# Kernel optimization log

Hardware: AMD Instinct MI355X
Metric: run time of the kernel (lower is better)

Reference implementation:

```python
import jax, jax.numpy as jnp
import numpy as np

B, CIN, COUT, K, L = 16, 512, 512, 3, 8192
STRIDE, PAD, DIL = 1, 1, 1  # 'same' conv: Lout == L


def setup_inputs() -> dict:
    key = jax.random.key(0)
    k1, k2, k3 = jax.random.split(key, 3)
    x = jax.random.normal(k1, (B, CIN, L), dtype=jnp.float32)
    # int8 quantized weight stored as int32 for portability; values in [-128, 127]
    qweight = jax.random.randint(k2, (COUT, CIN, K), -128, 128, dtype=jnp.int32)
    scale = jnp.float32(0.01)  # per-tensor dequant scale (w_max / 127)
    bias = jax.random.normal(k3, (COUT,), dtype=jnp.float32)
    return {"x": x, "qweight": qweight, "scale": scale, "bias": bias}


def reference(x, qweight, scale, bias):
    # Dequantize: fp32 weight = int8 * scale (materialized every call, as in torch module)
    w = (qweight.astype(jnp.float32) * scale).astype(x.dtype)
    out = jax.lax.conv_general_dilated(
        x, w,
        window_strides=(STRIDE,),
        padding=[(PAD, PAD)],
        rhs_dilation=(DIL,),
        dimension_numbers=("NCH", "OIH", "NCH"),
        feature_group_count=1,
    )
    return out + bias.astype(x.dtype)[None, :, None]
```

## Files before the change

### kernel.cpp

```cpp
#include <hip/hip_runtime.h>
#include <hip/hip_bf16.h>

#define CIN   512
#define COUT  512
#define LEN   8192
#define NB    16
#define KW    3
#define PROWS 8200

#define WB_ELEMS (COUT * CIN * KW)
#define WB_BYTES ((size_t)WB_ELEMS * 2)
#define XS_BYTES ((size_t)NB * PROWS * CIN * 2)

#define BM2 256
#define BN2 256
#define BK3 64
#define NT  ((CIN / BK3) * KW)
#define TILE3 (BM2 * BK3 * 2)

typedef __attribute__((ext_vector_type(4))) float f32x4;
typedef __attribute__((ext_vector_type(8))) short bf16x8;

static __device__ __forceinline__ unsigned short f2bf(float f) {
    union { float f; unsigned u; } cv; cv.f = f;
    return (unsigned short)((cv.u + 0x7fffu + ((cv.u >> 16) & 1u)) >> 16);
}

__global__ __launch_bounds__(256) void wconv_kernel(const int* __restrict__ q,
                                                    unsigned short* __restrict__ wb) {
    int idx = blockIdx.x * 256 + threadIdx.x;
    if (idx >= WB_ELEMS) return;
    int co = idx / (KW * CIN);
    int r  = idx - co * (KW * CIN);
    int t  = r >> 9;
    int ci = r & 511;
    wb[idx] = f2bf((float)q[(co * CIN + ci) * KW + t]);
}

__global__ __launch_bounds__(256) void zpad_kernel(unsigned short* __restrict__ xs) {
    int i = blockIdx.x * 256 + threadIdx.x;
    if (i >= NB * 2 * CIN) return;
    int b  = i >> 10;
    int r  = (i >> 9) & 1;
    int ci = i & 511;
    size_t p = (size_t)b * PROWS + (r ? 8193 : 0);
    xs[p * CIN + ci] = 0;
}

__global__ __launch_bounds__(256) void xprep_kernel(const float* __restrict__ x,
                                                    unsigned short* __restrict__ xs) {
    __shared__ char T[64 * 132];
    int blk = blockIdx.x;
    int b   = blk >> 10;
    int ci0 = ((blk >> 7) & 7) * 64;
    int l0  = (blk & 127) * 64;
    int tid = threadIdx.x;

    const float* src = x + ((size_t)b * CIN + ci0) * LEN + l0;
    for (int i = tid; i < 64 * 16; i += 256) {
        int r = i >> 4, c4 = i & 15;
        f32x4 v = *(const f32x4*)(src + (size_t)r * LEN + c4 * 4);
        unsigned lo = (unsigned)f2bf(v[0]) | ((unsigned)f2bf(v[1]) << 16);
        unsigned hi = (unsigned)f2bf(v[2]) | ((unsigned)f2bf(v[3]) << 16);
        char* p = T + r * 132 + c4 * 8;
        *(unsigned*)p       = lo;
        *(unsigned*)(p + 4) = hi;
    }
    __syncthreads();
    unsigned short* dst = xs + ((size_t)b * PROWS + 1 + l0) * CIN + ci0;
    for (int i = tid; i < 64 * 8; i += 256) {
        int l = i >> 3, c8 = i & 7;
        union { bf16x8 v; unsigned short s[8]; } pk;
        #pragma unroll
        for (int j = 0; j < 8; ++j)
            pk.s[j] = *(const unsigned short*)(T + (c8 * 8 + j) * 132 + l * 2);
        *(bf16x8*)(dst + (size_t)l * CIN + c8 * 8) = pk.v;
    }
}

__global__ __launch_bounds__(512, 2) void conv_kernel(
    const unsigned short* __restrict__ xs,
    const unsigned short* __restrict__ wb,
    const float* __restrict__ scale_p,
    const float* __restrict__ bias,
    float* __restrict__ out)
{
    __shared__ char sA[2][TILE3];
    __shared__ char sB[2][TILE3];

    const int bid = blockIdx.x;
    const int logical = (bid & 7) * 128 + (bid >> 3);
    const int co_tile = logical & 1;
    const int l_tile  = logical >> 1;
    const int b   = l_tile >> 5;
    const int l0  = (l_tile & 31) * BN2;
    const int co0 = co_tile * BM2;

    const int tid  = threadIdx.x;
    const int lane = tid & 63;
    const int wid  = tid >> 6;
    const int wr   = wid >> 2;
    const int wc   = wid & 3;
    const int lhi  = lane >> 4;
    const int llo  = lane & 15;

    f32x4 acc[8][4] = {};

    const char* xsB = (const char*)(xs + ((size_t)b * PROWS + l0) * CIN);
    const char* wbB = (const char*)wb + (size_t)co0 * (KW * CIN * 2);

#define STAGEU(buf_, c_, u_) do {                                                            \
    int tap_ = (c_) % KW;  int ci0_ = ((c_) / KW) * BK3;                                     \
    int rowoff_ = ((u_) & 1) * 128;                                                          \
    const char* src0_; size_t rstride_; char* dst0_;                                         \
    if ((u_) < 2) { src0_ = xsB + ((size_t)(tap_ + rowoff_) * CIN + ci0_) * 2;               \
                    rstride_ = CIN * 2; dst0_ = &sB[buf_][rowoff_ * 128]; }                   \
    else          { src0_ = wbB + (size_t)rowoff_ * (KW * CIN * 2)                           \
                            + ((size_t)tap_ * CIN + ci0_) * 2;                               \
                    rstride_ = KW * CIN * 2; dst0_ = &sA[buf_][rowoff_ * 128]; }             \
    _Pragma("unroll")                                                                        \
    for (int kk_ = 0; kk_ < 2; ++kk_) {                                                      \
        int it_ = tid + kk_ * 512;                                                           \
        int r_ = it_ >> 3, q_ = it_ & 7;                                                     \
        __builtin_amdgcn_global_load_lds(                                                    \
            (const __attribute__((address_space(1))) unsigned int*)                          \
                (src0_ + (size_t)r_ * rstride_ + ((q_ * 16) ^ ((r_ & 7) << 4))),             \
            (__attribute__((address_space(3))) unsigned int*)(dst0_ + it_ * 16),             \
            16, 0, 0);                                                                       \
    } } while (0)

#define LDA(d_, buf_, mq_, k_) do { int row_ = (mq_) * 32 + wr * 16 + llo;                   \
    d_ = *(const bf16x8*)(&sA[buf_][0] + row_ * 128                                          \
                          + (((k_) * 64 + lhi * 16) ^ ((row_ & 7) << 4))); } while (0)
#define LDB(d_, buf_, n_, k_) do { int row_ = wc * 64 + (n_) * 16 + llo;                     \
    d_ = *(const bf16x8*)(&sB[buf_][0] + row_ * 128                                          \
                          + (((k_) * 64 + lhi * 16) ^ ((row_ & 7) << 4))); } while (0)

#define MFMA16(p_) do {                                                                      \
    __builtin_amdgcn_s_setprio(1);                                                           \
    acc[2*(p_)  ][0] = __builtin_amdgcn_mfma_f32_16x16x32_bf16(a0_, bB00, acc[2*(p_)  ][0],0,0,0); \
    acc[2*(p_)  ][1] = __builtin_amdgcn_mfma_f32_16x16x32_bf16(a0_, bB10, acc[2*(p_)  ][1],0,0,0); \
    acc[2*(p_)  ][2] = __builtin_amdgcn_mfma_f32_16x16x32_bf16(a0_, bB20, acc[2*(p_)  ][2],0,0,0); \
    acc[2*(p_)  ][3] = __builtin_amdgcn_mfma_f32_16x16x32_bf16(a0_, bB30, acc[2*(p_)  ][3],0,0,0); \
    acc[2*(p_)+1][0] = __builtin_amdgcn_mfma_f32_16x16x32_bf16(a2_, bB00, acc[2*(p_)+1][0],0,0,0); \
    acc[2*(p_)+1][1] = __builtin_amdgcn_mfma_f32_16x16x32_bf16(a2_, bB10, acc[2*(p_)+1][1],0,0,0); \
    acc[2*(p_)+1][2] = __builtin_amdgcn_mfma_f32_16x16x32_bf16(a2_, bB20, acc[2*(p_)+1][2],0,0,0); \
    acc[2*(p_)+1][3] = __builtin_amdgcn_mfma_f32_16x16x32_bf16(a2_, bB30, acc[2*(p_)+1][3],0,0,0); \
    acc[2*(p_)  ][0] = __builtin_amdgcn_mfma_f32_16x16x32_bf16(a1_, bB01, acc[2*(p_)  ][0],0,0,0); \
    acc[2*(p_)  ][1] = __builtin_amdgcn_mfma_f32_16x16x32_bf16(a1_, bB11, acc[2*(p_)  ][1],0,0,0); \
    acc[2*(p_)  ][2] = __builtin_amdgcn_mfma_f32_16x16x32_bf16(a1_, bB21, acc[2*(p_)  ][2],0,0,0); \
    acc[2*(p_)  ][3] = __builtin_amdgcn_mfma_f32_16x16x32_bf16(a1_, bB31, acc[2*(p_)  ][3],0,0,0); \
    acc[2*(p_)+1][0] = __builtin_amdgcn_mfma_f32_16x16x32_bf16(a3_, bB01, acc[2*(p_)+1][0],0,0,0); \
    acc[2*(p_)+1][1] = __builtin_amdgcn_mfma_f32_16x16x32_bf16(a3_, bB11, acc[2*(p_)+1][1],0,0,0); \
    acc[2*(p_)+1][2] = __builtin_amdgcn_mfma_f32_16x16x32_bf16(a3_, bB21, acc[2*(p_)+1][2],0,0,0); \
    acc[2*(p_)+1][3] = __builtin_amdgcn_mfma_f32_16x16x32_bf16(a3_, bB31, acc[2*(p_)+1][3],0,0,0); \
    __builtin_amdgcn_s_setprio(0);                                                           \
    } while (0)

#define BAR()    __builtin_amdgcn_s_barrier()
#define SCHED0() __builtin_amdgcn_sched_barrier(0)
#define LGKM0()  asm volatile("s_waitcnt lgkmcnt(0)" ::: "memory")

    STAGEU(0, 0, 0); STAGEU(0, 0, 1); STAGEU(0, 0, 2); STAGEU(0, 0, 3);
    asm volatile("s_waitcnt vmcnt(2)" ::: "memory");
    BAR();

    bf16x8 bB00, bB01, bB10, bB11, bB20, bB21, bB30, bB31;
    bf16x8 a0_, a1_, a2_, a3_;

    #pragma unroll 1
    for (int c = 0; c < NT - 1; ++c) {
        const int buf = c & 1, nb = buf ^ 1;
        SCHED0();
        LDB(bB00, buf, 0, 0); LDB(bB01, buf, 0, 1);
        LDB(bB10, buf, 1, 0); LDB(bB11, buf, 1, 1);
        LDB(bB20, buf, 2, 0); LDB(bB21, buf, 2, 1);
        LDB(bB30, buf, 3, 0); LDB(bB31, buf, 3, 1);
        LDA(a0_, buf, 0, 0); LDA(a1_, buf, 0, 1); LDA(a2_, buf, 1, 0); LDA(a3_, buf, 1, 1);
        STAGEU(nb, c + 1, 0);
        BAR(); LGKM0(); SCHED0();
        MFMA16(0);
        BAR();
        SCHED0();
        LDA(a0_, buf, 2, 0); LDA(a1_, buf, 2, 1); LDA(a2_, buf, 3, 0); LDA(a3_, buf, 3, 1);
        STAGEU(nb, c + 1, 1);
        asm volatile("s_waitcnt vmcnt(4)" ::: "memory");
        BAR(); LGKM0(); SCHED0();
        MFMA16(1);
        BAR();
        SCHED0();
        LDA(a0_, buf, 4, 0); LDA(a1_, buf, 4, 1); LDA(a2_, buf, 5, 0); LDA(a3_, buf, 5, 1);
        STAGEU(nb, c + 1, 2);
        BAR(); LGKM0(); SCHED0();
        MFMA16(2);
        BAR();
        SCHED0();
        LDA(a0_, buf, 6, 0); LDA(a1_, buf, 6, 1); LDA(a2_, buf, 7, 0); LDA(a3_, buf, 7, 1);
        STAGEU(nb, c + 1, 3);
        asm volatile("s_waitcnt vmcnt(2)" ::: "memory");
        BAR(); LGKM0(); SCHED0();
        MFMA16(3);
        BAR();
    }
    {
        const int buf = (NT - 1) & 1;
        SCHED0();
        LDB(bB00, buf, 0, 0); LDB(bB01, buf, 0, 1);
        LDB(bB10, buf, 1, 0); LDB(bB11, buf, 1, 1);
        LDB(bB20, buf, 2, 0); LDB(bB21, buf, 2, 1);
        LDB(bB30, buf, 3, 0); LDB(bB31, buf, 3, 1);
        LDA(a0_, buf, 0, 0); LDA(a1_, buf, 0, 1); LDA(a2_, buf, 1, 0); LDA(a3_, buf, 1, 1);
        BAR(); LGKM0(); SCHED0();
        MFMA16(0);
        BAR();
        SCHED0();
        LDA(a0_, buf, 2, 0); LDA(a1_, buf, 2, 1); LDA(a2_, buf, 3, 0); LDA(a3_, buf, 3, 1);
        asm volatile("s_waitcnt vmcnt(0)" ::: "memory");
        BAR(); LGKM0(); SCHED0();
        MFMA16(1);
        BAR();
        SCHED0();
        LDA(a0_, buf, 4, 0); LDA(a1_, buf, 4, 1); LDA(a2_, buf, 5, 0); LDA(a3_, buf, 5, 1);
        BAR(); LGKM0(); SCHED0();
        MFMA16(2);
        BAR();
        SCHED0();
        LDA(a0_, buf, 6, 0); LDA(a1_, buf, 6, 1); LDA(a2_, buf, 7, 0); LDA(a3_, buf, 7, 1);
        LGKM0(); SCHED0();
        MFMA16(3);
    }
#undef STAGEU
#undef LDA
#undef LDB
#undef MFMA16

    const float sc = scale_p[0];
    #pragma unroll
    for (int m = 0; m < 8; ++m) {
        #pragma unroll
        for (int j = 0; j < 4; ++j) {
            int co = co0 + m * 32 + wr * 16 + lhi * 4 + j;
            float bv = bias[co];
            size_t orow = ((size_t)b * COUT + co) * LEN + l0 + wc * 64;
            #pragma unroll
            for (int n = 0; n < 4; ++n)
                out[orow + n * 16 + llo] = sc * acc[m][n][j] + bv;
        }
    }
}

__global__ __launch_bounds__(256, 2) void conv_fb_kernel(
    const float* __restrict__ x,
    const unsigned short* __restrict__ wb,
    const float* __restrict__ scale_p,
    const float* __restrict__ bias,
    float* __restrict__ out)
{
    __shared__ char xT[132 * 128];
    const int bid = blockIdx.x;
    const int logical = (bid & 7) * 512 + (bid >> 3);
    const int co_tile = logical & 3;
    const int n_tile  = logical >> 2;
    const int b   = n_tile >> 6;
    const int l0  = (n_tile & 63) * 128;
    const int co0 = co_tile * 128;
    const int tid  = threadIdx.x;
    const int lane = tid & 63;
    const int wid  = tid >> 6;
    const int wr = wid >> 1, wc = wid & 1;
    const int lhi = lane >> 4;
    const int llo = lane & 15;
    f32x4 acc[4][4] = {};
    const float* xb = x + (size_t)b * CIN * LEN;

    for (int ci0 = 0; ci0 < CIN; ci0 += 64) {
        __syncthreads();
        for (int it = tid; it < 132 * 8; it += 256) {
            int c = it % 132;
            int o = it / 132;
            int l = l0 - 1 + c;
            float v[8];
            if (l >= 0 && l < LEN) {
                const float* src = xb + (size_t)(ci0 + o * 8) * LEN + l;
                #pragma unroll
                for (int j = 0; j < 8; ++j) v[j] = src[(size_t)j * LEN];
            } else {
                #pragma unroll
                for (int j = 0; j < 8; ++j) v[j] = 0.f;
            }
            union { bf16x8 v8; unsigned short s[8]; } pk;
            #pragma unroll
            for (int j = 0; j < 8; ++j) pk.s[j] = f2bf(v[j]);
            int byte = c * 128 + ((o * 16) ^ ((c & 7) << 4));
            *reinterpret_cast<bf16x8*>(xT + byte) = pk.v8;
        }
        __syncthreads();
        #pragma unroll
        for (int t = 0; t < KW; ++t) {
            #pragma unroll
            for (int s = 0; s < 2; ++s) {
                bf16x8 af[4];
                #pragma unroll
                for (int m = 0; m < 4; ++m)
                    af[m] = *reinterpret_cast<const bf16x8*>(
                        wb + (size_t)(co0 + wr * 64 + m * 16 + llo) * (KW * CIN)
                           + t * CIN + ci0 + s * 32 + 8 * lhi);
                bf16x8 bfr[4];
                #pragma unroll
                for (int n = 0; n < 4; ++n) {
                    int col = wc * 64 + n * 16 + llo + t;
                    int byte = col * 128 + (((s * 32 + 8 * lhi) * 2) ^ ((col & 7) << 4));
                    bfr[n] = *reinterpret_cast<const bf16x8*>(xT + byte);
                }
                #pragma unroll
                for (int m = 0; m < 4; ++m)
                    #pragma unroll
                    for (int n = 0; n < 4; ++n)
                        acc[m][n] = __builtin_amdgcn_mfma_f32_16x16x32_bf16(af[m], bfr[n], acc[m][n], 0, 0, 0);
            }
        }
    }
    const float sc = scale_p[0];
    #pragma unroll
    for (int m = 0; m < 4; ++m) {
        #pragma unroll
        for (int j = 0; j < 4; ++j) {
            int co = co0 + wr * 64 + m * 16 + lhi * 4 + j;
            float bv = bias[co];
            size_t orow = ((size_t)b * COUT + co) * LEN + l0 + wc * 64;
            #pragma unroll
            for (int n = 0; n < 4; ++n)
                out[orow + n * 16 + llo] = sc * acc[m][n][j] + bv;
        }
    }
}

extern "C" void kernel_launch(void* const* d_in, const int* in_sizes, int n_in,
                              void* d_out, int out_size, void* d_ws, size_t ws_size,
                              hipStream_t stream) {
    const float* x    = (const float*)d_in[0];
    const int*   qw   = (const int*)d_in[1];
    const float* sc   = (const float*)d_in[2];
    const float* bias = (const float*)d_in[3];
    float* out = (float*)d_out;
    unsigned short* wb = (unsigned short*)d_ws;

    wconv_kernel<<<(WB_ELEMS + 255) / 256, 256, 0, stream>>>(qw, wb);

    if (ws_size >= WB_BYTES + XS_BYTES) {
        unsigned short* xsw = (unsigned short*)((char*)d_ws + WB_BYTES);
        zpad_kernel<<<(NB * 2 * CIN + 255) / 256, 256, 0, stream>>>(xsw);
        xprep_kernel<<<NB * 8 * (LEN / 64), 256, 0, stream>>>(x, xsw);
        conv_kernel<<<(COUT / BM2) * (NB * LEN / BN2), 512, 0, stream>>>(xsw, wb, sc, bias, out);
    } else {
        conv_fb_kernel<<<4096, 256, 0, stream>>>(x, wb, sc, bias, out);
    }
}
```

Measured before the change: 297.4 us.

## Precompute swizzled LDS/global addresses, reorder MFMA K-halves, fold zero-pad into xprep

The conv main loop now precomputes per-thread global and LDS pointers with the XOR swizzle folded in once, and advances them by constant deltas per K-step instead of recomputing addresses in every stage. MFMA issue is reordered so each phase processes one K-half (32 elements) against four A fragments, which reduces live B registers from eight to a reusable set. The separate zero-padding kernel is removed and its writes are folded into xprep, saving one launch. The aim is lower VALU address overhead and register pressure in the hot loop, but the pointer-stepping arithmetic for tap wraparound must stay exactly correct.

```diff
diff --git a/kernel.cpp b/kernel.cpp
--- a/kernel.cpp
+++ b/kernel.cpp
@@ -37,16 +37,6 @@
     wb[idx] = f2bf((float)q[(co * CIN + ci) * KW + t]);
 }
 
-__global__ __launch_bounds__(256) void zpad_kernel(unsigned short* __restrict__ xs) {
-    int i = blockIdx.x * 256 + threadIdx.x;
-    if (i >= NB * 2 * CIN) return;
-    int b  = i >> 10;
-    int r  = (i >> 9) & 1;
-    int ci = i & 511;
-    size_t p = (size_t)b * PROWS + (r ? 8193 : 0);
-    xs[p * CIN + ci] = 0;
-}
-
 __global__ __launch_bounds__(256) void xprep_kernel(const float* __restrict__ x,
                                                     unsigned short* __restrict__ xs) {
     __shared__ char T[64 * 132];
@@ -55,6 +45,11 @@
     int ci0 = ((blk >> 7) & 7) * 64;
     int l0  = (blk & 127) * 64;
     int tid = threadIdx.x;
+
+    if (l0 == 0 && tid < 64)
+        xs[((size_t)b * PROWS + 0) * CIN + ci0 + tid] = 0;
+    if (l0 == (LEN - 64) && tid < 64)
+        xs[((size_t)b * PROWS + (LEN + 1)) * CIN + ci0 + tid] = 0;
 
     const float* src = x + ((size_t)b * CIN + ci0) * LEN + l0;
     for (int i = tid; i < 64 * 16; i += 256) {
@@ -109,51 +104,59 @@
     const char* xsB = (const char*)(xs + ((size_t)b * PROWS + l0) * CIN);
     const char* wbB = (const char*)wb + (size_t)co0 * (KW * CIN * 2);
 
-#define STAGEU(buf_, c_, u_) do {                                                            \
-    int tap_ = (c_) % KW;  int ci0_ = ((c_) / KW) * BK3;                                     \
-    int rowoff_ = ((u_) & 1) * 128;                                                          \
-    const char* src0_; size_t rstride_; char* dst0_;                                         \
-    if ((u_) < 2) { src0_ = xsB + ((size_t)(tap_ + rowoff_) * CIN + ci0_) * 2;               \
-                    rstride_ = CIN * 2; dst0_ = &sB[buf_][rowoff_ * 128]; }                   \
-    else          { src0_ = wbB + (size_t)rowoff_ * (KW * CIN * 2)                           \
-                            + ((size_t)tap_ * CIN + ci0_) * 2;                               \
-                    rstride_ = KW * CIN * 2; dst0_ = &sA[buf_][rowoff_ * 128]; }             \
-    _Pragma("unroll")                                                                        \
-    for (int kk_ = 0; kk_ < 2; ++kk_) {                                                      \
-        int it_ = tid + kk_ * 512;                                                           \
-        int r_ = it_ >> 3, q_ = it_ & 7;                                                     \
-        __builtin_amdgcn_global_load_lds(                                                    \
-            (const __attribute__((address_space(1))) unsigned int*)                          \
-                (src0_ + (size_t)r_ * rstride_ + ((q_ * 16) ^ ((r_ & 7) << 4))),             \
-            (__attribute__((address_space(3))) unsigned int*)(dst0_ + it_ * 16),             \
-            16, 0, 0);                                                                       \
-    } } while (0)
-
-#define LDA(d_, buf_, mq_, k_) do { int row_ = (mq_) * 32 + wr * 16 + llo;                   \
-    d_ = *(const bf16x8*)(&sA[buf_][0] + row_ * 128                                          \
-                          + (((k_) * 64 + lhi * 16) ^ ((row_ & 7) << 4))); } while (0)
-#define LDB(d_, buf_, n_, k_) do { int row_ = wc * 64 + (n_) * 16 + llo;                     \
-    d_ = *(const bf16x8*)(&sB[buf_][0] + row_ * 128                                          \
-                          + (((k_) * 64 + lhi * 16) ^ ((row_ & 7) << 4))); } while (0)
-
-#define MFMA16(p_) do {                                                                      \
+    const int it0 = tid, it1 = tid + 512;
+    const int r0 = it0 >> 3, r1 = it1 >> 3;
+    const int sw0 = ((it0 & 7) * 16) ^ ((r0 & 7) << 4);
+    const int sw1 = ((it1 & 7) * 16) ^ ((r1 & 7) << 4);
+    const char* pBs[4] = { xsB + r0 * 1024 + sw0,          xsB + r1 * 1024 + sw1,
+                           xsB + (128 + r0) * 1024 + sw0,  xsB + (128 + r1) * 1024 + sw1 };
+    const char* pAs[4] = { wbB + (size_t)r0 * 3072 + sw0,         wbB + (size_t)r1 * 3072 + sw1,
+                           wbB + (size_t)(128 + r0) * 3072 + sw0, wbB + (size_t)(128 + r1) * 3072 + sw1 };
+    const int d0 = tid * 16, d1 = d0 + 8192;
+
+    const int s10 = llo & 3, s2 = (llo >> 2) & 1;
+    const int constA = (wr * 16 + llo) * 128 + ((lhi ^ s10) << 4);
+    const int constB = (wc * 64 + llo) * 128 + ((lhi ^ s10) << 4);
+    const char* pA0b = &sA[0][0] + constA + (s2 ? 64 : 0);
+    const char* pA1b = &sA[0][0] + constA + (s2 ? 0 : 64);
+    const char* pB0b = &sB[0][0] + constB + (s2 ? 64 : 0);
+    const char* pB1b = &sB[0][0] + constB + (s2 ? 0 : 64);
+
+#define STAGEU(buf_, u_) do {                                                                \
+    const char* s0_; const char* s1_; char* dd_;                                             \
+    if ((u_) == 0)      { s0_ = pBs[0]; s1_ = pBs[1]; dd_ = &sB[buf_][0];     }              \
+    else if ((u_) == 1) { s0_ = pBs[2]; s1_ = pBs[3]; dd_ = &sB[buf_][16384]; }              \
+    else if ((u_) == 2) { s0_ = pAs[0]; s1_ = pAs[1]; dd_ = &sA[buf_][0];     }              \
+    else                { s0_ = pAs[2]; s1_ = pAs[3]; dd_ = &sA[buf_][16384]; }              \
+    __builtin_amdgcn_global_load_lds(                                                        \
+        (const __attribute__((address_space(1))) unsigned int*)s0_,                          \
+        (__attribute__((address_space(3))) unsigned int*)(dd_ + d0), 16, 0, 0);              \
+    __builtin_amdgcn_global_load_lds(                                                        \
+        (const __attribute__((address_space(1))) unsigned int*)s1_,                          \
+        (__attribute__((address_space(3))) unsigned int*)(dd_ + d1), 16, 0, 0);              \
+    } while (0)
+
+#define RDA(p_, mq_) (*(const bf16x8*)((p_) + (mq_) * 4096))
+#define RDB(p_, n_)  (*(const bf16x8*)((p_) + (n_) * 2048))
+
+#define MFMA16(mb_, B0_, B1_, B2_, B3_) do {                                                 \
     __builtin_amdgcn_s_setprio(1);                                                           \
-    acc[2*(p_)  ][0] = __builtin_amdgcn_mfma_f32_16x16x32_bf16(a0_, bB00, acc[2*(p_)  ][0],0,0,0); \
-    acc[2*(p_)  ][1] = __builtin_amdgcn_mfma_f32_16x16x32_bf16(a0_, bB10, acc[2*(p_)  ][1],0,0,0); \
-    acc[2*(p_)  ][2] = __builtin_amdgcn_mfma_f32_16x16x32_bf16(a0_, bB20, acc[2*(p_)  ][2],0,0,0); \
-    acc[2*(p_)  ][3] = __builtin_amdgcn_mfma_f32_16x16x32_bf16(a0_, bB30, acc[2*(p_)  ][3],0,0,0); \
-    acc[2*(p_)+1][0] = __builtin_amdgcn_mfma_f32_16x16x32_bf16(a2_, bB00, acc[2*(p_)+1][0],0,0,0); \
-    acc[2*(p_)+1][1] = __builtin_amdgcn_mfma_f32_16x16x32_bf16(a2_, bB10, acc[2*(p_)+1][1],0,0,0); \
-    acc[2*(p_)+1][2] = __builtin_amdgcn_mfma_f32_16x16x32_bf16(a2_, bB20, acc[2*(p_)+1][2],0,0,0); \
-    acc[2*(p_)+1][3] = __builtin_amdgcn_mfma_f32_16x16x32_bf16(a2_, bB30, acc[2*(p_)+1][3],0,0,0); \
-    acc[2*(p_)  ][0] = __builtin_amdgcn_mfma_f32_16x16x32_bf16(a1_, bB01, acc[2*(p_)  ][0],0,0,0); \
-    acc[2*(p_)  ][1] = __builtin_amdgcn_mfma_f32_16x16x32_bf16(a1_, bB11, acc[2*(p_)  ][1],0,0,0); \
-    acc[2*(p_)  ][2] = __builtin_amdgcn_mfma_f32_16x16x32_bf16(a1_, bB21, acc[2*(p_)  ][2],0,0,0); \
-    acc[2*(p_)  ][3] = __builtin_amdgcn_mfma_f32_16x16x32_bf16(a1_, bB31, acc[2*(p_)  ][3],0,0,0); \
-    acc[2*(p_)+1][0] = __builtin_amdgcn_mfma_f32_16x16x32_bf16(a3_, bB01, acc[2*(p_)+1][0],0,0,0); \
-    acc[2*(p_)+1][1] = __builtin_amdgcn_mfma_f32_16x16x32_bf16(a3_, bB11, acc[2*(p_)+1][1],0,0,0); \
-    acc[2*(p_)+1][2] = __builtin_amdgcn_mfma_f32_16x16x32_bf16(a3_, bB21, acc[2*(p_)+1][2],0,0,0); \
-    acc[2*(p_)+1][3] = __builtin_amdgcn_mfma_f32_16x16x32_bf16(a3_, bB31, acc[2*(p_)+1][3],0,0,0); \
+    acc[(mb_)+0][0] = __builtin_amdgcn_mfma_f32_16x16x32_bf16(a0_, B0_, acc[(mb_)+0][0],0,0,0); \
+    acc[(mb_)+0][1] = __builtin_amdgcn_mfma_f32_16x16x32_bf16(a0_, B1_, acc[(mb_)+0][1],0,0,0); \
+    acc[(mb_)+0][2] = __builtin_amdgcn_mfma_f32_16x16x32_bf16(a0_, B2_, acc[(mb_)+0][2],0,0,0); \
+    acc[(mb_)+0][3] = __builtin_amdgcn_mfma_f32_16x16x32_bf16(a0_, B3_, acc[(mb_)+0][3],0,0,0); \
+    acc[(mb_)+1][0] = __builtin_amdgcn_mfma_f32_16x16x32_bf16(a1_, B0_, acc[(mb_)+1][0],0,0,0); \
+    acc[(mb_)+1][1] = __builtin_amdgcn_mfma_f32_16x16x32_bf16(a1_, B1_, acc[(mb_)+1][1],0,0,0); \
+    acc[(mb_)+1][2] = __builtin_amdgcn_mfma_f32_16x16x32_bf16(a1_, B2_, acc[(mb_)+1][2],0,0,0); \
+    acc[(mb_)+1][3] = __builtin_amdgcn_mfma_f32_16x16x32_bf16(a1_, B3_, acc[(mb_)+1][3],0,0,0); \
+    acc[(mb_)+2][0] = __builtin_amdgcn_mfma_f32_16x16x32_bf16(a2_, B0_, acc[(mb_)+2][0],0,0,0); \
+    acc[(mb_)+2][1] = __builtin_amdgcn_mfma_f32_16x16x32_bf16(a2_, B1_, acc[(mb_)+2][1],0,0,0); \
+    acc[(mb_)+2][2] = __builtin_amdgcn_mfma_f32_16x16x32_bf16(a2_, B2_, acc[(mb_)+2][2],0,0,0); \
+    acc[(mb_)+2][3] = __builtin_amdgcn_mfma_f32_16x16x32_bf16(a2_, B3_, acc[(mb_)+2][3],0,0,0); \
+    acc[(mb_)+3][0] = __builtin_amdgcn_mfma_f32_16x16x32_bf16(a3_, B0_, acc[(mb_)+3][0],0,0,0); \
+    acc[(mb_)+3][1] = __builtin_amdgcn_mfma_f32_16x16x32_bf16(a3_, B1_, acc[(mb_)+3][1],0,0,0); \
+    acc[(mb_)+3][2] = __builtin_amdgcn_mfma_f32_16x16x32_bf16(a3_, B2_, acc[(mb_)+3][2],0,0,0); \
+    acc[(mb_)+3][3] = __builtin_amdgcn_mfma_f32_16x16x32_bf16(a3_, B3_, acc[(mb_)+3][3],0,0,0); \
     __builtin_amdgcn_s_setprio(0);                                                           \
     } while (0)
 
@@ -161,77 +164,94 @@
 #define SCHED0() __builtin_amdgcn_sched_barrier(0)
 #define LGKM0()  asm volatile("s_waitcnt lgkmcnt(0)" ::: "memory")
 
-    STAGEU(0, 0, 0); STAGEU(0, 0, 1); STAGEU(0, 0, 2); STAGEU(0, 0, 3);
+    STAGEU(0, 0); STAGEU(0, 1); STAGEU(0, 2); STAGEU(0, 3);
+    {
+        #pragma unroll
+        for (int i = 0; i < 4; ++i) { pBs[i] += 1024; pAs[i] += 1024; }
+    }
+    int tapn = 1;
     asm volatile("s_waitcnt vmcnt(2)" ::: "memory");
     BAR();
 
-    bf16x8 bB00, bB01, bB10, bB11, bB20, bB21, bB30, bB31;
     bf16x8 a0_, a1_, a2_, a3_;
+    bf16x8 bk00, bk01, bk02, bk03;
+    bf16x8 bk10, bk11, bk12, bk13;
 
     #pragma unroll 1
     for (int c = 0; c < NT - 1; ++c) {
         const int buf = c & 1, nb = buf ^ 1;
-        SCHED0();
-        LDB(bB00, buf, 0, 0); LDB(bB01, buf, 0, 1);
-        LDB(bB10, buf, 1, 0); LDB(bB11, buf, 1, 1);
-        LDB(bB20, buf, 2, 0); LDB(bB21, buf, 2, 1);
-        LDB(bB30, buf, 3, 0); LDB(bB31, buf, 3, 1);
-        LDA(a0_, buf, 0, 0); LDA(a1_, buf, 0, 1); LDA(a2_, buf, 1, 0); LDA(a3_, buf, 1, 1);
-        STAGEU(nb, c + 1, 0);
-        BAR(); LGKM0(); SCHED0();
-        MFMA16(0);
-        BAR();
-        SCHED0();
-        LDA(a0_, buf, 2, 0); LDA(a1_, buf, 2, 1); LDA(a2_, buf, 3, 0); LDA(a3_, buf, 3, 1);
-        STAGEU(nb, c + 1, 1);
+        const int bufo = buf << 15;
+        const char* cpA0 = pA0b + bufo;
+        const char* cpA1 = pA1b + bufo;
+        const char* cpB0 = pB0b + bufo;
+        const char* cpB1 = pB1b + bufo;
+
+        SCHED0();
+        bk00 = RDB(cpB0, 0); bk01 = RDB(cpB0, 1); bk02 = RDB(cpB0, 2); bk03 = RDB(cpB0, 3);
+        a0_ = RDA(cpA0, 0); a1_ = RDA(cpA0, 1); a2_ = RDA(cpA0, 2); a3_ = RDA(cpA0, 3);
+        STAGEU(nb, 0);
+        BAR(); LGKM0(); SCHED0();
+        MFMA16(0, bk00, bk01, bk02, bk03);
+        BAR();
+        SCHED0();
+        bk10 = RDB(cpB1, 0); bk11 = RDB(cpB1, 1); bk12 = RDB(cpB1, 2); bk13 = RDB(cpB1, 3);
+        a0_ = RDA(cpA1, 0); a1_ = RDA(cpA1, 1); a2_ = RDA(cpA1, 2); a3_ = RDA(cpA1, 3);
+        STAGEU(nb, 1);
         asm volatile("s_waitcnt vmcnt(4)" ::: "memory");
         BAR(); LGKM0(); SCHED0();
-        MFMA16(1);
-        BAR();
-        SCHED0();
-        LDA(a0_, buf, 4, 0); LDA(a1_, buf, 4, 1); LDA(a2_, buf, 5, 0); LDA(a3_, buf, 5, 1);
-        STAGEU(nb, c + 1, 2);
-        BAR(); LGKM0(); SCHED0();
-        MFMA16(2);
-        BAR();
-        SCHED0();
-        LDA(a0_, buf, 6, 0); LDA(a1_, buf, 6, 1); LDA(a2_, buf, 7, 0); LDA(a3_, buf, 7, 1);
-        STAGEU(nb, c + 1, 3);
+        MFMA16(0, bk10, bk11, bk12, bk13);
+        BAR();
+        SCHED0();
+        a0_ = RDA(cpA0, 4); a1_ = RDA(cpA0, 5); a2_ = RDA(cpA0, 6); a3_ = RDA(cpA0, 7);
+        STAGEU(nb, 2);
+        BAR(); LGKM0(); SCHED0();
+        MFMA16(4, bk00, bk01, bk02, bk03);
+        BAR();
+        SCHED0();
+        a0_ = RDA(cpA1, 4); a1_ = RDA(cpA1, 5); a2_ = RDA(cpA1, 6); a3_ = RDA(cpA1, 7);
+        STAGEU(nb, 3);
         asm volatile("s_waitcnt vmcnt(2)" ::: "memory");
         BAR(); LGKM0(); SCHED0();
-        MFMA16(3);
-        BAR();
+        MFMA16(4, bk10, bk11, bk12, bk13);
+        BAR();
+
+        const int kd = (tapn == 2) ? -1920 : 1024;
+        tapn = (tapn == 2) ? 0 : tapn + 1;
+        #pragma unroll
+        for (int i = 0; i < 4; ++i) { pBs[i] += kd; pAs[i] += kd; }
     }
     {
-        const int buf = (NT - 1) & 1;
-        SCHED0();
-        LDB(bB00, buf, 0, 0); LDB(bB01, buf, 0, 1);
-        LDB(bB10, buf, 1, 0); LDB(bB11, buf, 1, 1);
-        LDB(bB20, buf, 2, 0); LDB(bB21, buf, 2, 1);
-        LDB(bB30, buf, 3, 0); LDB(bB31, buf, 3, 1);
-        LDA(a0_, buf, 0, 0); LDA(a1_, buf, 0, 1); LDA(a2_, buf, 1, 0); LDA(a3_, buf, 1, 1);
-        BAR(); LGKM0(); SCHED0();
-        MFMA16(0);
-        BAR();
-        SCHED0();
-        LDA(a0_, buf, 2, 0); LDA(a1_, buf, 2, 1); LDA(a2_, buf, 3, 0); LDA(a3_, buf, 3, 1);
+        const int bufo = ((NT - 1) & 1) << 15;
+        const char* cpA0 = pA0b + bufo;
+        const char* cpA1 = pA1b + bufo;
+        const char* cpB0 = pB0b + bufo;
+        const char* cpB1 = pB1b + bufo;
+        SCHED0();
+        bk00 = RDB(cpB0, 0); bk01 = RDB(cpB0, 1); bk02 = RDB(cpB0, 2); bk03 = RDB(cpB0, 3);
+        a0_ = RDA(cpA0, 0); a1_ = RDA(cpA0, 1); a2_ = RDA(cpA0, 2); a3_ = RDA(cpA0, 3);
+        BAR(); LGKM0(); SCHED0();
+        MFMA16(0, bk00, bk01, bk02, bk03);
+        BAR();
+        SCHED0();
+        bk10 = RDB(cpB1, 0); bk11 = RDB(cpB1, 1); bk12 = RDB(cpB1, 2); bk13 = RDB(cpB1, 3);
+        a0_ = RDA(cpA1, 0); a1_ = RDA(cpA1, 1); a2_ = RDA(cpA1, 2); a3_ = RDA(cpA1, 3);
         asm volatile("s_waitcnt vmcnt(0)" ::: "memory");
         BAR(); LGKM0(); SCHED0();
-        MFMA16(1);
-        BAR();
-        SCHED0();
-        LDA(a0_, buf, 4, 0); LDA(a1_, buf, 4, 1); LDA(a2_, buf, 5, 0); LDA(a3_, buf, 5, 1);
-        BAR(); LGKM0(); SCHED0();
-        MFMA16(2);
-        BAR();
-        SCHED0();
-        LDA(a0_, buf, 6, 0); LDA(a1_, buf, 6, 1); LDA(a2_, buf, 7, 0); LDA(a3_, buf, 7, 1);
+        MFMA16(0, bk10, bk11, bk12, bk13);
+        BAR();
+        SCHED0();
+        a0_ = RDA(cpA0, 4); a1_ = RDA(cpA0, 5); a2_ = RDA(cpA0, 6); a3_ = RDA(cpA0, 7);
+        BAR(); LGKM0(); SCHED0();
+        MFMA16(4, bk00, bk01, bk02, bk03);
+        BAR();
+        SCHED0();
+        a0_ = RDA(cpA1, 4); a1_ = RDA(cpA1, 5); a2_ = RDA(cpA1, 6); a3_ = RDA(cpA1, 7);
         LGKM0(); SCHED0();
-        MFMA16(3);
+        MFMA16(4, bk10, bk11, bk12, bk13);
     }
 #undef STAGEU
-#undef LDA
-#undef LDB
+#undef RDA
+#undef RDB
 #undef MFMA16
 
     const float sc = scale_p[0];
@@ -349,7 +369,6 @@
 
     if (ws_size >= WB_BYTES + XS_BYTES) {
         unsigned short* xsw = (unsigned short*)((char*)d_ws + WB_BYTES);
-        zpad_kernel<<<(NB * 2 * CIN + 255) / 256, 256, 0, stream>>>(xsw);
         xprep_kernel<<<NB * 8 * (LEN / 64), 256, 0, stream>>>(x, xsw);
         conv_kernel<<<(COUT / BM2) * (NB * LEN / BN2), 512, 0, stream>>>(xsw, wb, sc, bias, out);
     } else {
```

Measured after the change: 301.1 us. No clear change (+1.3%).
